# Kernel tuning notes

Hardware: AMD Instinct MI355X
Metric: run time of the kernel (lower is better)

## Reference

```python
import jax, jax.numpy as jnp
import numpy as np

IN_FEATURES = 8192
OUT_FEATURES = 8192
CODESZ = 8            # E8 lattice dimension per code index
CODEBOOK_SIZE = 65536 # 2^16-entry codebook (16-bit indices)
TOKENS = 32           # decode-style batch


def fwht(x):
    """Fast Walsh-Hadamard transform (Sylvester order) along the last axis.
    n must be a power of 2. Unnormalized (multiply by H_n)."""
    n = x.shape[-1]
    steps = int(np.log2(n))
    h = 1
    for _ in range(steps):
        y = x.reshape(*x.shape[:-1], n // (2 * h), 2, h)
        a = y[..., 0, :]
        b = y[..., 1, :]
        x = jnp.stack([a + b, a - b], axis=-2).reshape(*y.shape[:-3], n)
        h *= 2
    return x


def setup_inputs() -> dict:
    key = jax.random.key(0)
    k0, k1, k2, k3, k4 = jax.random.split(key, 5)
    x = jax.random.normal(k0, (TOKENS, IN_FEATURES), dtype=jnp.float32)
    # learned codebook: CODEBOOK_SIZE vectors of CODESZ entries (E8P-like lattice points)
    codebook_table = jax.random.normal(k1, (CODEBOOK_SIZE, CODESZ), dtype=jnp.float32) * 0.1
    # quantized weight indices: [out_features, in_features // codesz]
    Qidxs = jax.random.randint(k2, (OUT_FEATURES, IN_FEATURES // CODESZ), 0, CODEBOOK_SIZE, dtype=jnp.int32)
    # random sign vectors (incoherence processing)
    SU = (2.0 * jax.random.randint(k3, (IN_FEATURES,), 0, 2) - 1.0).astype(jnp.float32)
    SV = (2.0 * jax.random.randint(k4, (OUT_FEATURES,), 0, 2) - 1.0).astype(jnp.float32)
    Wscale = jnp.array(0.02, dtype=jnp.float32)
    return {"x": x, "codebook_table": codebook_table, "Qidxs": Qidxs,
            "SU": SU, "SV": SV, "Wscale": Wscale}


def reference(x, codebook_table, Qidxs, SU, SV, Wscale):
    n_in = x.shape[-1]
    n_out = SV.shape[0]
    # input incoherence: sign flip then orthonormal Hadamard rotation (matmul_hadUt)
    xh = fwht(x * SU) * (1.0 / jnp.sqrt(jnp.float32(n_in)))  # [T, n_in]
    # codebook dequantization: gather lattice vectors and lay out as [n_out, n_in]
    W = codebook_table[Qidxs].reshape(n_out, n_in)
    # quantized matmul in the rotated basis
    z = xh @ W.T  # [T, n_out]
    # output rotation (matmul_hadU) + sign/scale (SV absorbs Wscale in the torch code)
    out = fwht(z) * (1.0 / jnp.sqrt(jnp.float32(n_out))) * (SV * Wscale)
    return out
```

## Files before the change

kernel.cpp:

```cpp
#include <hip/hip_runtime.h>
#include <hip/hip_bf16.h>


typedef __attribute__((ext_vector_type(16))) float f32x16;
typedef __attribute__((ext_vector_type(8))) __bf16 bf16x8;
typedef __attribute__((ext_vector_type(4))) __bf16 bf16x4;
typedef __attribute__((ext_vector_type(4))) int i32x4;

#define IN_F 8192
#define OUT_F 8192
#define TOKENS 32
#define KSPLIT 16
#define KCHUNK 512
#define CH (KCHUNK / 8)
#define DG 5
#define DI 7
#define INV_SQRT_8192 0.011048543456039806f
#define PAD(i) ((i) + ((i) >> 5))

#if __has_builtin(__builtin_amdgcn_raw_buffer_load_b128) && \
    __has_builtin(__builtin_amdgcn_make_buffer_rsrc)
#define HAVE_BUF 1
#else
#define HAVE_BUF 0
#endif

__device__ inline void fwht32_reg(float* r) {
    #pragma unroll
    for (int h = 1; h < 32; h <<= 1)
        #pragma unroll
        for (int i = 0; i < 32; i += 2 * h)
            #pragma unroll
            for (int j = 0; j < h; ++j) {
                float a = r[i + j], b = r[i + j + h];
                r[i + j] = a + b;
                r[i + j + h] = a - b;
            }
}

__device__ inline void fwht8192_lds(float* s, int tid) {
    float r[32];
    int b1 = tid * 32;
    #pragma unroll
    for (int j = 0; j < 32; ++j) r[j] = s[PAD(b1 + j)];
    fwht32_reg(r);
    #pragma unroll
    for (int j = 0; j < 32; ++j) s[PAD(b1 + j)] = r[j];
    __syncthreads();
    int b2 = (tid & 31) + (tid >> 5) * 1024;
    #pragma unroll
    for (int j = 0; j < 32; ++j) r[j] = s[PAD(b2 + 32 * j)];
    fwht32_reg(r);
    #pragma unroll
    for (int j = 0; j < 32; ++j) s[PAD(b2 + 32 * j)] = r[j];
    __syncthreads();
    #pragma unroll
    for (int jj = 0; jj < 4; ++jj) {
        float g[8];
        int b3 = tid * 4 + jj;
        #pragma unroll
        for (int k = 0; k < 8; ++k) g[k] = s[PAD(b3 + 1024 * k)];
        #pragma unroll
        for (int h = 1; h < 8; h <<= 1)
            #pragma unroll
            for (int i = 0; i < 8; i += 2 * h)
                #pragma unroll
                for (int j = 0; j < h; ++j) {
                    float a = g[i + j], b = g[i + j + h];
                    g[i + j] = a + b;
                    g[i + j + h] = a - b;
                }
        #pragma unroll
        for (int k = 0; k < 8; ++k) s[PAD(b3 + 1024 * k)] = g[k];
    }
    __syncthreads();
}

__global__ __launch_bounds__(256)
void prep_kernel(const float* __restrict__ cb, __bf16* __restrict__ cbb,
                 const float* __restrict__ x, const float* __restrict__ su,
                 __bf16* __restrict__ xh) {
    __shared__ float s[8192 + 256];
    const int tid = threadIdx.x;
    if (blockIdx.x < 512) {
        int i = blockIdx.x * 256 + tid;
        float4 v = ((const float4*)cb)[i];
        bf16x4 o;
        o[0] = (__bf16)v.x; o[1] = (__bf16)v.y;
        o[2] = (__bf16)v.z; o[3] = (__bf16)v.w;
        ((bf16x4*)cbb)[i] = o;
        return;
    }
    const int t = blockIdx.x - 512;
    #pragma unroll
    for (int i = tid; i < IN_F; i += 256)
        s[PAD(i)] = x[t * IN_F + i] * su[i];
    __syncthreads();
    fwht8192_lds(s, tid);
    #pragma unroll
    for (int i = tid; i < IN_F; i += 256)
        xh[t * IN_F + i] = (__bf16)(s[PAD(i)] * INV_SQRT_8192);
}

__global__ __launch_bounds__(512, 4)
void qgemm_kernel(const int* __restrict__ qidxs,
                  const __bf16* __restrict__ cb,
                  const __bf16* __restrict__ xh,
                  __bf16* __restrict__ zpart) {
    __shared__ __align__(16) __bf16 xt[TOKENS * KCHUNK];
    const int ks = blockIdx.x & 15;
    const int nb = blockIdx.x >> 4;
    const int tid = threadIdx.x;
    const int wave = tid >> 6, lane = tid & 63;
    const int h = lane >> 5, lc = lane & 31;
    const int n = nb * 256 + wave * 32 + lc;

    #pragma unroll
    for (int i = 0; i < 4; ++i) {
        int f = i * 512 + tid, r = f >> 6, c = f & 63;
        i32x4 v = *(const i32x4*)(xh + (size_t)r * IN_F + ks * KCHUNK + c * 8);
        *(i32x4*)(xt + ((r * CH + (c ^ (r & 7))) << 3)) = v;
    }
    __syncthreads();

    const int* qrow = qidxs + (size_t)n * (IN_F / 8) + ks * CH;

#if HAVE_BUF
    __amdgpu_buffer_rsrc_t rsrc = __builtin_amdgcn_make_buffer_rsrc(
        (void*)cb, (short)0, 65536 * 16, 0x00020000);
    #define GATHER(ix) __builtin_bit_cast(bf16x8, \
        __builtin_amdgcn_raw_buffer_load_b128(rsrc, (ix) << 4, 0, 1))
#else
    const bf16x8* cbv = (const bf16x8*)cb;
    #define GATHER(ix) (cbv[ix])
#endif

    f32x16 acc;
    #pragma unroll
    for (int i = 0; i < 16; ++i) acc[i] = 0.f;

    i32x4 iv[16];
    bf16x8 bfr[16][2];

    #pragma unroll
    for (int g = 0; g < DI; ++g)
        iv[g] = *(const i32x4*)(qrow + g * 4);
    #pragma unroll
    for (int g = 0; g < DG; ++g) {
        bfr[g][0] = GATHER(h ? iv[g][1] : iv[g][0]);
        bfr[g][1] = GATHER(h ? iv[g][3] : iv[g][2]);
    }

    #pragma unroll
    for (int g = 0; g < 16; ++g) {
        if (g + DI < 16)
            iv[g + DI] = *(const i32x4*)(qrow + (g + DI) * 4);
        if (g + DG < 16) {
            bfr[g + DG][0] = GATHER(h ? iv[g + DG][1] : iv[g + DG][0]);
            bfr[g + DG][1] = GATHER(h ? iv[g + DG][3] : iv[g + DG][2]);
        }
        #pragma unroll
        for (int sgi = 0; sgi < 2; ++sgi) {
            const int T = 2 * g + sgi;
            bf16x8 a = *(const bf16x8*)(xt +
                          ((lc * CH + ((2 * T + h) ^ (lc & 7))) << 3));
            acc = __builtin_amdgcn_mfma_f32_32x32x16_bf16(a, bfr[g][sgi],
                                                          acc, 0, 0, 0);
        }
    }

    __bf16* zp = zpart + ((size_t)ks * TOKENS) * OUT_F + n;
    #pragma unroll
    for (int r = 0; r < 16; ++r) {
        int m = (r & 3) + 4 * h + 8 * (r >> 2);
        zp[(size_t)m * OUT_F] = (__bf16)acc[r];
    }
}

__global__ __launch_bounds__(256)
void zsum_kernel(const __bf16* __restrict__ zpart, const float* __restrict__ sv,
                 const float* __restrict__ wscale, float* __restrict__ out) {
    __shared__ float s[8192 + 256];
    const int t = blockIdx.x, tid = threadIdx.x;
    #pragma unroll
    for (int cc = 0; cc < 4; ++cc) {
        int col = cc * 2048 + tid * 8;
        float a[8] = {0.f, 0.f, 0.f, 0.f, 0.f, 0.f, 0.f, 0.f};
        #pragma unroll
        for (int ks = 0; ks < KSPLIT; ++ks) {
            bf16x8 v = *(const bf16x8*)(zpart +
                         ((size_t)(ks * TOKENS + t)) * OUT_F + col);
            #pragma unroll
            for (int j = 0; j < 8; ++j) a[j] += (float)v[j];
        }
        #pragma unroll
        for (int j = 0; j < 8; ++j) s[PAD(col + j)] = a[j];
    }
    __syncthreads();
    fwht8192_lds(s, tid);
    const float sc = INV_SQRT_8192 * wscale[0];
    #pragma unroll
    for (int i = tid; i < OUT_F; i += 256)
        out[t * OUT_F + i] = s[PAD(i)] * sc * sv[i];
}

extern "C" void kernel_launch(void* const* d_in, const int* in_sizes, int n_in,
                              void* d_out, int out_size, void* d_ws, size_t ws_size,
                              hipStream_t stream) {
    const float* x      = (const float*)d_in[0];
    const float* cb     = (const float*)d_in[1];
    const int*   qidxs  = (const int*)d_in[2];
    const float* su     = (const float*)d_in[3];
    const float* sv     = (const float*)d_in[4];
    const float* wscale = (const float*)d_in[5];
    float* out = (float*)d_out;

    char* ws = (char*)d_ws;
    __bf16* cb_bf16 = (__bf16*)ws;
    __bf16* xh      = (__bf16*)(ws + (1u << 20));
    __bf16* zpart   = (__bf16*)(ws + (1u << 20) + (512u << 10));

    hipLaunchKernelGGL(prep_kernel, dim3(544), dim3(256), 0, stream,
                       cb, cb_bf16, x, su, xh);
    hipLaunchKernelGGL(qgemm_kernel, dim3(32 * KSPLIT), dim3(512), 0, stream,
                       qidxs, cb_bf16, xh, zpart);
    hipLaunchKernelGGL(zsum_kernel, dim3(TOKENS), dim3(256), 0, stream,
                       zpart, sv, wscale, out);
}
```

Baseline: 138.5 us.

## Halve K-split to 8 with 1024-wide chunks and alternate gather cache policy

Doubles the K chunk each qgemm block covers (KSPLIT 16→8), halving the number of blocks, the bf16 partial-sum traffic, and the reduction work in zsum. Each block now stages 64KB of activations in LDS and runs twice as many gather/MFMA groups. Codebook gathers now alternate between aux cache policy 0 and 1 on even and odd groups, to vary the caching behaviour of the random codebook lookups. The larger LDS footprint and longer per-block loop may reduce occupancy and latency hiding.

After: 133.9 us. -3.3%, faster.

```diff
diff --git a/kernel.cpp b/kernel.cpp
--- a/kernel.cpp
+++ b/kernel.cpp
@@ -10,9 +10,10 @@
 #define IN_F 8192
 #define OUT_F 8192
 #define TOKENS 32
-#define KSPLIT 16
-#define KCHUNK 512
+#define KSPLIT 8
+#define KCHUNK 1024
 #define CH (KCHUNK / 8)
+#define GROUPS (KCHUNK / 32)
 #define DG 5
 #define DI 7
 #define INV_SQRT_8192 0.011048543456039806f
@@ -108,56 +109,66 @@
                   const __bf16* __restrict__ xh,
                   __bf16* __restrict__ zpart) {
     __shared__ __align__(16) __bf16 xt[TOKENS * KCHUNK];
-    const int ks = blockIdx.x & 15;
-    const int nb = blockIdx.x >> 4;
+    const int ks = blockIdx.x & (KSPLIT - 1);
+    const int nb = blockIdx.x >> 3;
     const int tid = threadIdx.x;
     const int wave = tid >> 6, lane = tid & 63;
     const int h = lane >> 5, lc = lane & 31;
     const int n = nb * 256 + wave * 32 + lc;
 
     #pragma unroll
-    for (int i = 0; i < 4; ++i) {
-        int f = i * 512 + tid, r = f >> 6, c = f & 63;
+    for (int i = 0; i < 8; ++i) {
+        int f = i * 512 + tid, r = f >> 7, c = f & 127;
         i32x4 v = *(const i32x4*)(xh + (size_t)r * IN_F + ks * KCHUNK + c * 8);
         *(i32x4*)(xt + ((r * CH + (c ^ (r & 7))) << 3)) = v;
     }
     __syncthreads();
 
-    const int* qrow = qidxs + (size_t)n * (IN_F / 8) + ks * CH;
+    const int* qrow = qidxs + (size_t)n * (IN_F / 8) + ks * (KCHUNK / 8);
 
 #if HAVE_BUF
     __amdgpu_buffer_rsrc_t rsrc = __builtin_amdgcn_make_buffer_rsrc(
         (void*)cb, (short)0, 65536 * 16, 0x00020000);
-    #define GATHER(ix) __builtin_bit_cast(bf16x8, \
-        __builtin_amdgcn_raw_buffer_load_b128(rsrc, (ix) << 4, 0, 1))
+    #define GA(ix, au) __builtin_bit_cast(bf16x8, \
+        __builtin_amdgcn_raw_buffer_load_b128(rsrc, (ix) << 4, 0, au))
 #else
     const bf16x8* cbv = (const bf16x8*)cb;
-    #define GATHER(ix) (cbv[ix])
+    #define GA(ix, au) (cbv[ix])
 #endif
 
     f32x16 acc;
     #pragma unroll
     for (int i = 0; i < 16; ++i) acc[i] = 0.f;
 
-    i32x4 iv[16];
-    bf16x8 bfr[16][2];
+    i32x4 iv[GROUPS];
+    bf16x8 bfr[GROUPS][2];
 
     #pragma unroll
     for (int g = 0; g < DI; ++g)
         iv[g] = *(const i32x4*)(qrow + g * 4);
     #pragma unroll
     for (int g = 0; g < DG; ++g) {
-        bfr[g][0] = GATHER(h ? iv[g][1] : iv[g][0]);
-        bfr[g][1] = GATHER(h ? iv[g][3] : iv[g][2]);
-    }
-
-    #pragma unroll
-    for (int g = 0; g < 16; ++g) {
-        if (g + DI < 16)
+        if (g & 1) {
+            bfr[g][0] = GA(h ? iv[g][1] : iv[g][0], 1);
+            bfr[g][1] = GA(h ? iv[g][3] : iv[g][2], 1);
+        } else {
+            bfr[g][0] = GA(h ? iv[g][1] : iv[g][0], 0);
+            bfr[g][1] = GA(h ? iv[g][3] : iv[g][2], 0);
+        }
+    }
+
+    #pragma unroll
+    for (int g = 0; g < GROUPS; ++g) {
+        if (g + DI < GROUPS)
             iv[g + DI] = *(const i32x4*)(qrow + (g + DI) * 4);
-        if (g + DG < 16) {
-            bfr[g + DG][0] = GATHER(h ? iv[g + DG][1] : iv[g + DG][0]);
-            bfr[g + DG][1] = GATHER(h ? iv[g + DG][3] : iv[g + DG][2]);
+        if (g + DG < GROUPS) {
+            if ((g + DG) & 1) {
+                bfr[g + DG][0] = GA(h ? iv[g + DG][1] : iv[g + DG][0], 1);
+                bfr[g + DG][1] = GA(h ? iv[g + DG][3] : iv[g + DG][2], 1);
+            } else {
+                bfr[g + DG][0] = GA(h ? iv[g + DG][1] : iv[g + DG][0], 0);
+                bfr[g + DG][1] = GA(h ? iv[g + DG][3] : iv[g + DG][2], 0);
+            }
         }
         #pragma unroll
         for (int sgi = 0; sgi < 2; ++sgi) {
```
